# Performance work log

Hardware: AMD Instinct MI355X
Metric: run time of the kernel (lower is better)

## Reference

```python
import jax, jax.numpy as jnp
import numpy as np
from jax import lax

D = 1024      # hidden_dim
H = 1408      # moe_inter_dim
E = 8         # num_experts
K = 2         # topk
ROUTER_SCALE = 1.0


def setup_inputs() -> dict:
    key = jax.random.key(0)
    ks = jax.random.split(key, 16)
    s = 0.02
    inp = {
        "x": jax.random.normal(ks[0], (2, 2048, D), dtype=jnp.float32),
        "gate_w": jax.random.normal(ks[1], (E, D), dtype=jnp.float32) * s,
        "gate_b": jax.random.normal(ks[2], (E,), dtype=jnp.float32) * s,
        # stacked expert params; torch Linear weight [out,in] stored transposed as [in,out]
        "w1": jax.random.normal(ks[3], (E, D, H), dtype=jnp.float32) * s,
        "b1": jax.random.normal(ks[4], (E, H), dtype=jnp.float32) * s,
        "w3": jax.random.normal(ks[5], (E, D, H), dtype=jnp.float32) * s,
        "b3": jax.random.normal(ks[6], (E, H), dtype=jnp.float32) * s,
        "w2": jax.random.normal(ks[7], (E, H, D), dtype=jnp.float32) * s,
        "b2": jax.random.normal(ks[8], (E, D), dtype=jnp.float32) * s,
        # shared expert
        "sw1": jax.random.normal(ks[9], (D, H), dtype=jnp.float32) * s,
        "sb1": jax.random.normal(ks[10], (H,), dtype=jnp.float32) * s,
        "sw3": jax.random.normal(ks[11], (D, H), dtype=jnp.float32) * s,
        "sb3": jax.random.normal(ks[12], (H,), dtype=jnp.float32) * s,
        "sw2": jax.random.normal(ks[13], (H, D), dtype=jnp.float32) * s,
        "sb2": jax.random.normal(ks[14], (D,), dtype=jnp.float32) * s,
    }
    return inp


def _expert(x, w1, b1, w3, b3, w2, b2):
    # NOTE: source applies silu to the PRODUCT: w2(silu(w1(x) * w3(x)))
    h = jax.nn.silu((x @ w1 + b1) * (x @ w3 + b3))
    return h @ w2 + b2


def reference(x, gate_w, gate_b, w1, b1, w3, b3, w2, b2,
              sw1, sb1, sw3, sb3, sw2, sb2):
    shape = x.shape
    xf = x.reshape(-1, D)                      # [T, D]
    T = xf.shape[0]

    # Gate
    scores = jax.nn.softmax(xf @ gate_w.T, axis=-1)   # [T, E]
    biased = scores + gate_b
    _, idx = lax.top_k(biased, K)                     # [T, K] int32
    w = jnp.take_along_axis(scores, idx, axis=-1) * ROUTER_SCALE  # [T, K]

    # Dense routing-weight matrix (top-k indices are distinct per token)
    rw = jnp.zeros((T, E), dtype=xf.dtype).at[jnp.arange(T)[:, None], idx].add(w)

    # Stacked expert compute: [T, E, H] -> [T, E, D], combined by routing weight
    h = jax.nn.silu((jnp.einsum('td,edh->teh', xf, w1) + b1)
                    * (jnp.einsum('td,edh->teh', xf, w3) + b3))
    oe = jnp.einsum('teh,ehd->ted', h, w2) + b2
    y = jnp.einsum('te,ted->td', rw, oe)

    # Shared expert on all tokens
    z = _expert(xf, sw1, sb1, sw3, sb3, sw2, sb2)
    return (y + z).reshape(shape)
```

## Files before the change

### kernel.cpp

```cpp
#include <hip/hip_runtime.h>
#include <math.h>

#define DD 1024
#define HH 1408
#define NE 8

typedef __attribute__((ext_vector_type(8))) __bf16 bf16x8;
typedef __attribute__((ext_vector_type(4))) float f32x4;

__device__ __forceinline__ float bf2f(unsigned short u) {
  union { unsigned int i; float f; } v; v.i = ((unsigned int)u) << 16; return v.f;
}
__device__ __forceinline__ unsigned short f2bf(float f) {
  union { float f; unsigned int i; } v; v.f = f;
  unsigned int r = v.i + 0x7FFFu + ((v.i >> 16) & 1u);
  return (unsigned short)(r >> 16);
}
__device__ __forceinline__ float tof(float f) { return f; }
__device__ __forceinline__ float tof(unsigned short u) { return bf2f(u); }

__device__ __forceinline__ void cvt2(float a, float b, unsigned int* o) {
  asm("v_cvt_pk_bf16_f32 %0, %1, %2" : "=v"(*o) : "v"(a), "v"(b));
}

__device__ __forceinline__ void ld8cvt(const float* p, unsigned int* o) {
  float4 a = *(const float4*)p;
  float4 b = *(const float4*)(p + 4);
  cvt2(a.x, a.y, o + 0); cvt2(a.z, a.w, o + 1);
  cvt2(b.x, b.y, o + 2); cvt2(b.z, b.w, o + 3);
}

typedef unsigned int __attribute__((address_space(1))) gu32;
typedef unsigned int __attribute__((address_space(3))) lu32;
__device__ __forceinline__ void gl16(const unsigned short* g, unsigned short* l) {
  __builtin_amdgcn_global_load_lds((const gu32*)g, (lu32*)l, 16, 0, 0);
}

__global__ void sniff_kernel(const unsigned short* __restrict__ xw,
                             int* __restrict__ dflag) {
  __shared__ int cnt;
  if (threadIdx.x == 0) cnt = 0;
  __syncthreads();
  unsigned short v = xw[threadIdx.x];
  int e = (v >> 7) & 0xFF;
  if (e >= 100 && e <= 140) atomicAdd(&cnt, 1);
  __syncthreads();
  if (threadIdx.x == 0) dflag[0] = (cnt < 230) ? 1 : 0;
}

__global__ void cvtx_kernel(const void* __restrict__ x,
                            const int* __restrict__ dflag,
                            unsigned short* __restrict__ xb, int n8) {
  int i = blockIdx.x * blockDim.x + threadIdx.x;
  int st = gridDim.x * blockDim.x;
  if (dflag[0]) {
    const float* xs = (const float*)x;
    for (; i < n8; i += st) {
      unsigned int o[4];
      ld8cvt(xs + (size_t)i * 8, o);
      *(uint4*)(xb + (size_t)i * 8) = *(uint4*)o;
    }
  } else {
    const uint4* xs = (const uint4*)x;
    for (; i < n8; i += st) *(uint4*)(xb + (size_t)i * 8) = xs[i];
  }
}

__global__ void trans_kernel(const void* __restrict__ wmain,
                             const void* __restrict__ wsh,
                             const int* __restrict__ dflag,
                             unsigned short* __restrict__ out, int R, int C) {
  __shared__ float tile[32][33];
  const int mat = blockIdx.z;
  const int r0 = blockIdx.y << 5, c0 = blockIdx.x << 5;
  const int t = threadIdx.x;
  const int lr = t >> 3, lc = (t & 7) << 2;
  const size_t mbase = (size_t)mat * R * C;
  if (dflag[0]) {
    const float* src = (mat < NE) ? ((const float*)wmain + mbase) : (const float*)wsh;
    float4 v = *(const float4*)(src + (size_t)(r0 + lr) * C + c0 + lc);
    tile[lr][lc] = v.x; tile[lr][lc + 1] = v.y;
    tile[lr][lc + 2] = v.z; tile[lr][lc + 3] = v.w;
  } else {
    const unsigned short* src = (mat < NE) ? ((const unsigned short*)wmain + mbase)
                                           : (const unsigned short*)wsh;
    ushort4 v = *(const ushort4*)(src + (size_t)(r0 + lr) * C + c0 + lc);
    tile[lr][lc] = bf2f(v.x); tile[lr][lc + 1] = bf2f(v.y);
    tile[lr][lc + 2] = bf2f(v.z); tile[lr][lc + 3] = bf2f(v.w);
  }
  __syncthreads();
  const int oc = t >> 3;
  const int orr = (t & 7) << 2;
  unsigned int p0, p1;
  cvt2(tile[orr][oc], tile[orr + 1][oc], &p0);
  cvt2(tile[orr + 2][oc], tile[orr + 3][oc], &p1);
  uint2 pk; pk.x = p0; pk.y = p1;
  *(uint2*)(out + mbase + (size_t)(c0 + oc) * R + r0 + orr) = pk;
}

__global__ void cvtb_kernel(const void* b1, const void* b3, const void* b2,
                            const void* sb1, const void* sb3, const void* sb2,
                            const int* __restrict__ dflag,
                            float* __restrict__ bf1, float* __restrict__ bf3,
                            float* __restrict__ bf2o) {
  int i = blockIdx.x * blockDim.x + threadIdx.x;
  const int nh = (NE + 1) * HH, nd = (NE + 1) * DD;
  const bool f32 = dflag[0] != 0;
  auto get = [&](const void* pm, const void* ps, int idx, int per) -> float {
    int mat = idx / per, j = idx - mat * per;
    if (f32) return (mat < NE) ? ((const float*)pm)[(size_t)mat * per + j]
                               : ((const float*)ps)[j];
    return bf2f((mat < NE) ? ((const unsigned short*)pm)[(size_t)mat * per + j]
                           : ((const unsigned short*)ps)[j]);
  };
  if (i < nh) bf1[i] = get(b1, sb1, i, HH);
  else if (i < 2 * nh) bf3[i - nh] = get(b3, sb3, i - nh, HH);
  else if (i < 2 * nh + nd) bf2o[i - 2 * nh] = get(b2, sb2, i - 2 * nh, DD);
}

template <class T>
__device__ void gate_body(const T* __restrict__ x,
                          const T* __restrict__ gw,
                          const T* __restrict__ gb,
                          int* __restrict__ tok_eidx,
                          float* __restrict__ tok_w, int T_) {
  int t = (int)((blockIdx.x * blockDim.x + threadIdx.x) >> 6);
  int lane = threadIdx.x & 63;
  if (t >= T_) return;
  const T* xr = x + (size_t)t * DD;
  float acc[NE];
#pragma unroll
  for (int e = 0; e < NE; e++) acc[e] = 0.f;
  for (int i = lane; i < DD; i += 64) {
    float xv = tof(xr[i]);
#pragma unroll
    for (int e = 0; e < NE; e++) acc[e] += xv * tof(gw[e * DD + i]);
  }
#pragma unroll
  for (int off = 32; off > 0; off >>= 1) {
#pragma unroll
    for (int e = 0; e < NE; e++) acc[e] += __shfl_xor(acc[e], off);
  }
  if (lane == 0) {
    float mx = acc[0];
#pragma unroll
    for (int e = 1; e < NE; e++) mx = fmaxf(mx, acc[e]);
    float s = 0.f, sc[NE], bi[NE];
#pragma unroll
    for (int e = 0; e < NE; e++) { sc[e] = expf(acc[e] - mx); s += sc[e]; }
    float inv = 1.f / s;
#pragma unroll
    for (int e = 0; e < NE; e++) { sc[e] *= inv; bi[e] = sc[e] + tof(gb[e]); }
    int i1 = 0;
#pragma unroll
    for (int e = 1; e < NE; e++) if (bi[e] > bi[i1]) i1 = e;
    int i2 = (i1 == 0) ? 1 : 0;
#pragma unroll
    for (int e = 0; e < NE; e++) if (e != i1 && bi[e] > bi[i2]) i2 = e;
    tok_eidx[t * 2] = i1; tok_eidx[t * 2 + 1] = i2;
    tok_w[t * 2] = sc[i1]; tok_w[t * 2 + 1] = sc[i2];
  }
}

__global__ void gate_kernel(const void* x, const void* gw, const void* gb,
                            const int* __restrict__ dflag,
                            int* tok_eidx, float* tok_w, int T_) {
  if (dflag[0])
    gate_body<float>((const float*)x, (const float*)gw, (const float*)gb,
                     tok_eidx, tok_w, T_);
  else
    gate_body<unsigned short>((const unsigned short*)x, (const unsigned short*)gw,
                              (const unsigned short*)gb, tok_eidx, tok_w, T_);
}

__global__ void prep_kernel(const int* __restrict__ tok_eidx,
                            const float* __restrict__ tok_w,
                            int* __restrict__ meta,
                            int* __restrict__ rows_tok,
                            float* __restrict__ rows_wgt,
                            int* __restrict__ tok_pos,
                            int t0, int TS) {
  __shared__ int cnt[NE];
  __shared__ int off[NE];
  const int tid = threadIdx.x;
  if (tid < NE) cnt[tid] = 0;
  __syncthreads();
  const int n2 = TS * 2;
  const int* te = tok_eidx + (size_t)t0 * 2;
  const float* tw = tok_w + (size_t)t0 * 2;
  for (int i = tid; i < n2; i += (int)blockDim.x) atomicAdd(&cnt[te[i]], 1);
  __syncthreads();
  if (tid == 0) {
    int s = 0;
#pragma unroll
    for (int e = 0; e < NE; e++) { off[e] = s; meta[16 + e] = s; s += cnt[e]; }
    meta[16 + NE] = s;
  }
  __syncthreads();
  for (int i = tid; i < n2; i += (int)blockDim.x) {
    int pos = atomicAdd(&off[te[i]], 1);
    rows_tok[pos] = t0 + (i >> 1);
    rows_wgt[pos] = tw[i];
    tok_pos[(size_t)(t0 + (i >> 1)) * 2 + (i & 1)] = pos;
  }
}

__global__ void combine_kernel(const float4* __restrict__ r_out,
                               const int* __restrict__ tok_pos,
                               float4* __restrict__ out, int t0, int TS) {
  const int C4 = DD / 4;
  int i = blockIdx.x * blockDim.x + threadIdx.x;
  int n4 = TS * C4;
  int st = gridDim.x * blockDim.x;
  for (; i < n4; i += st) {
    int tl = i / C4, c = i - tl * C4;
    int t = t0 + tl;
    int p0 = tok_pos[t * 2], p1 = tok_pos[t * 2 + 1];
    float4 a = out[(size_t)t * C4 + c];
    float4 b = r_out[(size_t)p0 * C4 + c];
    float4 d = r_out[(size_t)p1 * C4 + c];
    a.x += b.x + d.x; a.y += b.y + d.y;
    a.z += b.z + d.z; a.w += b.w + d.w;
    out[(size_t)t * C4 + c] = a;
  }
}

__global__ __launch_bounds__(512, 2)
void ffn_up_kernel(const unsigned short* __restrict__ xb,
                   const unsigned short* __restrict__ wt1,
                   const unsigned short* __restrict__ wt3,
                   const float* __restrict__ bf1, const float* __restrict__ bf3,
                   const int* __restrict__ meta,
                   const int* __restrict__ rows_tok,
                   unsigned short* __restrict__ h_buf,
                   unsigned short* __restrict__ sh_buf,
                   int t0, int TS, int my) {
  const int NX = HH / 128;
  const int P = NX * (NE + 1);
  const int id = blockIdx.x;
  const int xcd = id & 7;
  const int rest = id >> 3;
  const int mtile = rest % my;
  const int chunk = rest / my;
  const int panel = chunk * 8 + xcd;
  if (panel >= P) return;
  const int z = panel / NX;
  const int n0 = (panel - z * NX) * 128;

  const bool shx = (z == NE);
  int g0, cnt;
  unsigned short* ho;
  if (shx) { g0 = 0; cnt = TS; ho = sh_buf; }
  else {
    g0 = meta[16 + z]; cnt = meta[17 + z] - g0;
    ho = h_buf + (size_t)g0 * HH;
  }
  if (mtile * 256 >= cnt) return;
  const unsigned short* wa = wt1 + (size_t)z * HH * DD;
  const unsigned short* wb = wt3 + (size_t)z * HH * DD;

  __shared__ alignas(16) unsigned short lds[2 * 32768];

  const int tid = threadIdx.x;
  const int lane = tid & 63, wid = tid >> 6;
  const int rsub = wid * 8 + (lane >> 3);
  const int sl8 = (((lane & 7) ^ (lane >> 3)) << 3);

  size_t aoff[4];
#pragma unroll
  for (int c = 0; c < 4; c++) {
    int r = c * 64 + rsub;
    int m = mtile * 256 + r;
    int rr = (m < cnt) ? m : (cnt - 1);
    int srow = shx ? (t0 + rr) : rows_tok[g0 + rr];
    aoff[c] = (size_t)srow * DD + sl8;
  }
  size_t boff[2];
#pragma unroll
  for (int c = 0; c < 2; c++)
    boff[c] = (size_t)(n0 + c * 64 + rsub) * DD + sl8;

  const int ln15 = lane & 15;
  const int lg = lane >> 4;
  const int wr = (wid >> 1) << 6;
  const int wc = (wid & 1) << 6;
  const int ldsw = wid * 512;

  f32x4 acc1[4][4], acc3[4][4];
#pragma unroll
  for (int a = 0; a < 4; a++)
#pragma unroll
    for (int b = 0; b < 4; b++) {
      acc1[a][b] = {0.f, 0.f, 0.f, 0.f};
      acc3[a][b] = {0.f, 0.f, 0.f, 0.f};
    }

  auto stage = [&](int buf, int k) {
    unsigned short* Lb = &lds[buf * 32768];
#pragma unroll
    for (int c = 0; c < 4; c++)
      gl16(xb + aoff[c] + k, Lb + c * 4096 + ldsw);
#pragma unroll
    for (int c = 0; c < 2; c++) {
      gl16(wa + boff[c] + k, Lb + 16384 + c * 4096 + ldsw);
      gl16(wb + boff[c] + k, Lb + 24576 + c * 4096 + ldsw);
    }
  };

  stage(0, 0);
  const int NT = DD / 64;
  for (int t = 0; t < NT; ++t) {
    if (t + 1 < NT) {
      stage((t + 1) & 1, (t + 1) * 64);
      asm volatile("s_waitcnt vmcnt(8)" ::: "memory");
    } else {
      asm volatile("s_waitcnt vmcnt(0)" ::: "memory");
    }
    __builtin_amdgcn_sched_barrier(0);
    __builtin_amdgcn_s_barrier();
    __builtin_amdgcn_sched_barrier(0);
    const unsigned short* Lb = &lds[(t & 1) * 32768];
    __builtin_amdgcn_s_setprio(1);
#pragma unroll
    for (int ks = 0; ks < 2; ks++) {
      bf16x8 af[4];
#pragma unroll
      for (int fm = 0; fm < 4; fm++) {
        int R = wr + fm * 16 + ln15;
        af[fm] = *(const bf16x8*)&Lb[R * 64 + ((((ks << 2) | lg) ^ (R & 7)) << 3)];
      }
#pragma unroll
      for (int fn = 0; fn < 4; fn++) {
        int Rb = wc + fn * 16 + ln15;
        int o = Rb * 64 + ((((ks << 2) | lg) ^ (Rb & 7)) << 3);
        bf16x8 b1v = *(const bf16x8*)&Lb[16384 + o];
        bf16x8 b3v = *(const bf16x8*)&Lb[24576 + o];
#pragma unroll
        for (int fm = 0; fm < 4; fm++) {
          acc1[fm][fn] = __builtin_amdgcn_mfma_f32_16x16x32_bf16(af[fm], b1v, acc1[fm][fn], 0, 0, 0);
          acc3[fm][fn] = __builtin_amdgcn_mfma_f32_16x16x32_bf16(af[fm], b3v, acc3[fm][fn], 0, 0, 0);
        }
      }
    }
    __builtin_amdgcn_s_setprio(0);
    asm volatile("s_waitcnt lgkmcnt(0)" ::: "memory");
    __builtin_amdgcn_sched_barrier(0);
    __builtin_amdgcn_s_barrier();
    __builtin_amdgcn_sched_barrier(0);
  }

  const int kq4 = lg << 2;
#pragma unroll
  for (int fm = 0; fm < 4; fm++) {
#pragma unroll
    for (int r = 0; r < 4; r++) {
      int m = mtile * 256 + wr + fm * 16 + kq4 + r;
      if (m < cnt) {
        unsigned short* orow = ho + (size_t)m * HH + n0;
#pragma unroll
        for (int fn = 0; fn < 4; fn++) {
          int nc = wc + fn * 16 + ln15;
          float g1 = acc1[fm][fn][r] + bf1[(size_t)z * HH + n0 + nc];
          float g3 = acc3[fm][fn][r] + bf3[(size_t)z * HH + n0 + nc];
          float u = g1 * g3;
          float hv = u * __builtin_amdgcn_rcpf(1.f + __expf(-u));
          orow[nc] = f2bf(hv);
        }
      }
    }
  }
}

__global__ __launch_bounds__(512, 2)
void ffn_down_kernel(const unsigned short* __restrict__ h_buf,
                     const unsigned short* __restrict__ sh_buf,
                     const unsigned short* __restrict__ wt2,
                     const float* __restrict__ bf2,
                     const int* __restrict__ meta,
                     const int* __restrict__ rows_tok,
                     const float* __restrict__ rows_wgt,
                     float* __restrict__ r_out,
                     float* __restrict__ out, int t0, int TS, int my) {
  const int NX = DD / 128;
  const int P = NX * (NE + 1);
  const int id = blockIdx.x;
  const int xcd = id & 7;
  const int rest = id >> 3;
  const int mtile = rest % my;
  const int chunk = rest / my;
  const int panel = chunk * 8 + xcd;
  if (panel >= P) return;
  const int z = panel / NX;
  const int n0 = (panel - z * NX) * 128;

  const bool shx = (z == NE);
  int g0, cnt;
  const unsigned short* hb;
  if (shx) { g0 = 0; cnt = TS; hb = sh_buf; }
  else {
    g0 = meta[16 + z]; cnt = meta[17 + z] - g0;
    hb = h_buf + (size_t)g0 * HH;
  }
  if (mtile * 256 >= cnt) return;
  const unsigned short* ws = wt2 + (size_t)z * DD * HH;

  __shared__ alignas(16) unsigned short lds[2 * 24576];

  const int tid = threadIdx.x;
  const int lane = tid & 63, wid = tid >> 6;
  const int rsub = wid * 8 + (lane >> 3);
  const int sl8 = (((lane & 7) ^ (lane >> 3)) << 3);

  size_t aoff[4];
#pragma unroll
  for (int c = 0; c < 4; c++) {
    int r = c * 64 + rsub;
    int m = mtile * 256 + r;
    int rr = (m < cnt) ? m : (cnt - 1);
    aoff[c] = (size_t)rr * HH + sl8;
  }
  size_t boff[2];
#pragma unroll
  for (int c = 0; c < 2; c++)
    boff[c] = (size_t)(n0 + c * 64 + rsub) * HH + sl8;

  const int ln15 = lane & 15;
  const int lg = lane >> 4;
  const int wr = (wid >> 1) << 6;
  const int wc = (wid & 1) << 6;
  const int ldsw = wid * 512;

  f32x4 acc[4][4];
#pragma unroll
  for (int a = 0; a < 4; a++)
#pragma unroll
    for (int b = 0; b < 4; b++) acc[a][b] = {0.f, 0.f, 0.f, 0.f};

  auto stage = [&](int buf, int k) {
    unsigned short* Lb = &lds[buf * 24576];
#pragma unroll
    for (int c = 0; c < 4; c++)
      gl16(hb + aoff[c] + k, Lb + c * 4096 + ldsw);
#pragma unroll
    for (int c = 0; c < 2; c++)
      gl16(ws + boff[c] + k, Lb + 16384 + c * 4096 + ldsw);
  };

  stage(0, 0);
  const int NT = HH / 64;
  for (int t = 0; t < NT; ++t) {
    if (t + 1 < NT) {
      stage((t + 1) & 1, (t + 1) * 64);
      asm volatile("s_waitcnt vmcnt(6)" ::: "memory");
    } else {
      asm volatile("s_waitcnt vmcnt(0)" ::: "memory");
    }
    __builtin_amdgcn_sched_barrier(0);
    __builtin_amdgcn_s_barrier();
    __builtin_amdgcn_sched_barrier(0);
    const unsigned short* Lb = &lds[(t & 1) * 24576];
    __builtin_amdgcn_s_setprio(1);
#pragma unroll
    for (int ks = 0; ks < 2; ks++) {
      bf16x8 af[4];
#pragma unroll
      for (int fm = 0; fm < 4; fm++) {
        int R = wr + fm * 16 + ln15;
        af[fm] = *(const bf16x8*)&Lb[R * 64 + ((((ks << 2) | lg) ^ (R & 7)) << 3)];
      }
#pragma unroll
      for (int fn = 0; fn < 4; fn++) {
        int Rb = wc + fn * 16 + ln15;
        int o = Rb * 64 + ((((ks << 2) | lg) ^ (Rb & 7)) << 3);
        bf16x8 bv = *(const bf16x8*)&Lb[16384 + o];
#pragma unroll
        for (int fm = 0; fm < 4; fm++)
          acc[fm][fn] = __builtin_amdgcn_mfma_f32_16x16x32_bf16(af[fm], bv, acc[fm][fn], 0, 0, 0);
      }
    }
    __builtin_amdgcn_s_setprio(0);
    asm volatile("s_waitcnt lgkmcnt(0)" ::: "memory");
    __builtin_amdgcn_sched_barrier(0);
    __builtin_amdgcn_s_barrier();
    __builtin_amdgcn_sched_barrier(0);
  }

  const int kq4 = lg << 2;
#pragma unroll
  for (int fm = 0; fm < 4; fm++) {
#pragma unroll
    for (int r4 = 0; r4 < 4; r4++) {
      int m = mtile * 256 + wr + fm * 16 + kq4 + r4;
      if (m < cnt) {
        float* orow;
        float wgt;
        if (shx) { orow = out + (size_t)(t0 + m) * DD + n0; wgt = 1.f; }
        else { orow = r_out + (size_t)(g0 + m) * DD + n0; wgt = rows_wgt[g0 + m]; }
#pragma unroll
        for (int fn = 0; fn < 4; fn++) {
          int nc = wc + fn * 16 + ln15;
          orow[nc] = wgt * (acc[fm][fn][r4] + bf2[(size_t)z * DD + n0 + nc]);
        }
      }
    }
  }
}

extern "C" void kernel_launch(void* const* d_in, const int* in_sizes, int n_in,
                              void* d_out, int out_size, void* d_ws, size_t ws_size,
                              hipStream_t stream) {
  const void* x   = d_in[0];
  const void* gw  = d_in[1];
  const void* gb  = d_in[2];
  const void* w1  = d_in[3];
  const void* b1  = d_in[4];
  const void* w3  = d_in[5];
  const void* b3  = d_in[6];
  const void* w2  = d_in[7];
  const void* b2  = d_in[8];
  const void* sw1 = d_in[9];
  const void* sb1 = d_in[10];
  const void* sw3 = d_in[11];
  const void* sb3 = d_in[12];
  const void* sw2 = d_in[13];
  const void* sb2 = d_in[14];

  const int T = in_sizes[0] / DD;
  (void)n_in; (void)out_size;

  const size_t WMAT = (size_t)(NE + 1) * HH * DD;

  auto need = [&](int S) -> size_t {
    int TS = T / S;
    size_t o = 0;
    auto pad = [&](size_t b) { o = (o + b + 255) & ~(size_t)255; };
    pad(256);
    pad(32 * sizeof(int));
    pad((size_t)T * 2 * sizeof(int));
    pad((size_t)T * 2 * sizeof(float));
    pad((size_t)T * 2 * sizeof(int));
    pad((size_t)T * DD * 2);
    pad(WMAT * 2);
    pad(WMAT * 2);
    pad(WMAT * 2);
    pad((size_t)(NE + 1) * HH * sizeof(float));
    pad((size_t)(NE + 1) * HH * sizeof(float));
    pad((size_t)(NE + 1) * DD * sizeof(float));
    pad((size_t)TS * 2 * sizeof(int));
    pad((size_t)TS * 2 * sizeof(float));
    pad((size_t)TS * 2 * HH * 2);
    pad((size_t)TS * HH * 2);
    pad((size_t)TS * 2 * DD * sizeof(float));
    return o;
  };
  int S = 32;
  {
    const int cand[6] = {1, 2, 4, 8, 16, 32};
    for (int ci = 0; ci < 6; ci++) {
      if (need(cand[ci]) <= ws_size) { S = cand[ci]; break; }
    }
  }
  const int TS = T / S;
  const int my = (TS + 255) / 256;

  char* w = (char*)d_ws;
  size_t off = 0;
  auto take = [&](size_t bytes) {
    char* p = w + off;
    off = (off + bytes + 255) & ~(size_t)255;
    return p;
  };
  int*   dflag    = (int*)  take(256);
  int*   meta     = (int*)  take(32 * sizeof(int));
  int*   tok_eidx = (int*)  take((size_t)T * 2 * sizeof(int));
  float* tok_w    = (float*)take((size_t)T * 2 * sizeof(float));
  int*   tok_pos  = (int*)  take((size_t)T * 2 * sizeof(int));
  unsigned short* xb  = (unsigned short*)take((size_t)T * DD * 2);
  unsigned short* wt1 = (unsigned short*)take(WMAT * 2);
  unsigned short* wt3 = (unsigned short*)take(WMAT * 2);
  unsigned short* wt2 = (unsigned short*)take(WMAT * 2);
  float* bf1 = (float*)take((size_t)(NE + 1) * HH * sizeof(float));
  float* bf3 = (float*)take((size_t)(NE + 1) * HH * sizeof(float));
  float* bf2 = (float*)take((size_t)(NE + 1) * DD * sizeof(float));
  int*   rows_tok = (int*)  take((size_t)TS * 2 * sizeof(int));
  float* rows_wgt = (float*)take((size_t)TS * 2 * sizeof(float));
  unsigned short* h_buf  = (unsigned short*)take((size_t)TS * 2 * HH * 2);
  unsigned short* sh_buf = (unsigned short*)take((size_t)TS * HH * 2);
  float* r_out = (float*)take((size_t)TS * 2 * DD * sizeof(float));

  sniff_kernel<<<1, 256, 0, stream>>>((const unsigned short*)x, dflag);

  cvtx_kernel<<<2048, 256, 0, stream>>>(x, dflag, xb, T * DD / 8);
  trans_kernel<<<dim3(HH / 32, DD / 32, NE + 1), 256, 0, stream>>>(w1, sw1, dflag, wt1, DD, HH);
  trans_kernel<<<dim3(HH / 32, DD / 32, NE + 1), 256, 0, stream>>>(w3, sw3, dflag, wt3, DD, HH);
  trans_kernel<<<dim3(DD / 32, HH / 32, NE + 1), 256, 0, stream>>>(w2, sw2, dflag, wt2, HH, DD);
  {
    int nb = (2 * (NE + 1) * HH + (NE + 1) * DD + 255) / 256;
    cvtb_kernel<<<nb, 256, 0, stream>>>(b1, b3, b2, sb1, sb3, sb2, dflag, bf1, bf3, bf2);
  }

  gate_kernel<<<(T + 3) / 4, 256, 0, stream>>>(x, gw, gb, dflag, tok_eidx, tok_w, T);

  const int upP = (HH / 128) * (NE + 1);
  const int dnP = (DD / 128) * (NE + 1);
  const int upGrid = 8 * ((upP + 7) / 8) * my;
  const int dnGrid = 8 * ((dnP + 7) / 8) * my;

  for (int s = 0; s < S; s++) {
    const int t0 = s * TS;
    prep_kernel<<<1, 1024, 0, stream>>>(tok_eidx, tok_w, meta, rows_tok, rows_wgt,
                                        tok_pos, t0, TS);
    ffn_up_kernel<<<upGrid, 512, 0, stream>>>(
        xb, wt1, wt3, bf1, bf3, meta, rows_tok, h_buf, sh_buf, t0, TS, my);
    ffn_down_kernel<<<dnGrid, 512, 0, stream>>>(
        h_buf, sh_buf, wt2, bf2, meta, rows_tok, rows_wgt, r_out,
        (float*)d_out, t0, TS, my);
    combine_kernel<<<1024, 256, 0, stream>>>((const float4*)r_out, tok_pos,
                                             (float4*)d_out, t0, TS);
  }
}
```

Baseline: 454.5 us.

## Switch expert GEMMs to triple-buffered BK=32 pipeline with single barrier per step

Both expert GEMM kernels (gate/up and down) move from a double-buffered 64-wide K tile to a triple-buffered 32-wide K tile. Loads are issued two stages ahead, and each iteration now has one barrier instead of two. The LDS swizzle changes to match 32-element rows. The aim is to hide more global-load latency and cut LDS footprint for better occupancy, at the cost of twice as many loop iterations. The setprio and lgkmcnt waits are dropped, which relies on the three-buffer rotation to keep reads and writes from overlapping.

New measurement: 440.1 us. 3.2% less time.

```diff
diff --git a/kernel.cpp b/kernel.cpp
--- a/kernel.cpp
+++ b/kernel.cpp
@@ -259,32 +259,32 @@
   const unsigned short* wa = wt1 + (size_t)z * HH * DD;
   const unsigned short* wb = wt3 + (size_t)z * HH * DD;
 
-  __shared__ alignas(16) unsigned short lds[2 * 32768];
+  __shared__ alignas(16) unsigned short lds[3 * 16384];
 
   const int tid = threadIdx.x;
   const int lane = tid & 63, wid = tid >> 6;
-  const int rsub = wid * 8 + (lane >> 3);
-  const int sl8 = (((lane & 7) ^ (lane >> 3)) << 3);
-
-  size_t aoff[4];
-#pragma unroll
-  for (int c = 0; c < 4; c++) {
-    int r = c * 64 + rsub;
+
+  size_t aoff[2];
+#pragma unroll
+  for (int c = 0; c < 2; c++) {
+    int g = c * 512 + tid;
+    int r = g >> 2, s = g & 3;
     int m = mtile * 256 + r;
     int rr = (m < cnt) ? m : (cnt - 1);
     int srow = shx ? (t0 + rr) : rows_tok[g0 + rr];
-    aoff[c] = (size_t)srow * DD + sl8;
-  }
-  size_t boff[2];
-#pragma unroll
-  for (int c = 0; c < 2; c++)
-    boff[c] = (size_t)(n0 + c * 64 + rsub) * DD + sl8;
+    aoff[c] = (size_t)srow * DD + ((s ^ ((r >> 1) & 3)) << 3);
+  }
+  size_t boffs;
+  {
+    int rb = tid >> 2, sb = tid & 3;
+    boffs = (size_t)(n0 + rb) * DD + ((sb ^ ((rb >> 1) & 3)) << 3);
+  }
+  const int wbase = wid * 512;
 
   const int ln15 = lane & 15;
   const int lg = lane >> 4;
   const int wr = (wid >> 1) << 6;
   const int wc = (wid & 1) << 6;
-  const int ldsw = wid * 512;
 
   f32x4 acc1[4][4], acc3[4][4];
 #pragma unroll
@@ -296,57 +296,41 @@
     }
 
   auto stage = [&](int buf, int k) {
-    unsigned short* Lb = &lds[buf * 32768];
-#pragma unroll
-    for (int c = 0; c < 4; c++)
-      gl16(xb + aoff[c] + k, Lb + c * 4096 + ldsw);
-#pragma unroll
-    for (int c = 0; c < 2; c++) {
-      gl16(wa + boff[c] + k, Lb + 16384 + c * 4096 + ldsw);
-      gl16(wb + boff[c] + k, Lb + 24576 + c * 4096 + ldsw);
-    }
+    unsigned short* Lb = &lds[buf * 16384];
+#pragma unroll
+    for (int c = 0; c < 2; c++)
+      gl16(xb + aoff[c] + k, Lb + c * 4096 + wbase);
+    gl16(wa + boffs + k, Lb + 8192 + wbase);
+    gl16(wb + boffs + k, Lb + 12288 + wbase);
   };
 
+  const int NT = DD / 32;
   stage(0, 0);
-  const int NT = DD / 64;
+  stage(1, 32);
   for (int t = 0; t < NT; ++t) {
-    if (t + 1 < NT) {
-      stage((t + 1) & 1, (t + 1) * 64);
-      asm volatile("s_waitcnt vmcnt(8)" ::: "memory");
-    } else {
-      asm volatile("s_waitcnt vmcnt(0)" ::: "memory");
-    }
-    __builtin_amdgcn_sched_barrier(0);
-    __builtin_amdgcn_s_barrier();
-    __builtin_amdgcn_sched_barrier(0);
-    const unsigned short* Lb = &lds[(t & 1) * 32768];
-    __builtin_amdgcn_s_setprio(1);
-#pragma unroll
-    for (int ks = 0; ks < 2; ks++) {
-      bf16x8 af[4];
+    if (t + 1 < NT) asm volatile("s_waitcnt vmcnt(4)" ::: "memory");
+    else            asm volatile("s_waitcnt vmcnt(0)" ::: "memory");
+    asm volatile("s_barrier" ::: "memory");
+    if (t + 2 < NT) stage((t + 2) % 3, (t + 2) * 32);
+    const unsigned short* Lb = &lds[(t % 3) * 16384];
+    bf16x8 af[4];
+#pragma unroll
+    for (int fm = 0; fm < 4; fm++) {
+      int R = wr + fm * 16 + ln15;
+      af[fm] = *(const bf16x8*)&Lb[R * 32 + ((lg ^ ((R >> 1) & 3)) << 3)];
+    }
+#pragma unroll
+    for (int fn = 0; fn < 4; fn++) {
+      int Rb = wc + fn * 16 + ln15;
+      int o = Rb * 32 + ((lg ^ ((Rb >> 1) & 3)) << 3);
+      bf16x8 b1v = *(const bf16x8*)&Lb[8192 + o];
+      bf16x8 b3v = *(const bf16x8*)&Lb[12288 + o];
 #pragma unroll
       for (int fm = 0; fm < 4; fm++) {
-        int R = wr + fm * 16 + ln15;
-        af[fm] = *(const bf16x8*)&Lb[R * 64 + ((((ks << 2) | lg) ^ (R & 7)) << 3)];
+        acc1[fm][fn] = __builtin_amdgcn_mfma_f32_16x16x32_bf16(af[fm], b1v, acc1[fm][fn], 0, 0, 0);
+        acc3[fm][fn] = __builtin_amdgcn_mfma_f32_16x16x32_bf16(af[fm], b3v, acc3[fm][fn], 0, 0, 0);
       }
-#pragma unroll
-      for (int fn = 0; fn < 4; fn++) {
-        int Rb = wc + fn * 16 + ln15;
-        int o = Rb * 64 + ((((ks << 2) | lg) ^ (Rb & 7)) << 3);
-        bf16x8 b1v = *(const bf16x8*)&Lb[16384 + o];
-        bf16x8 b3v = *(const bf16x8*)&Lb[24576 + o];
-#pragma unroll
-        for (int fm = 0; fm < 4; fm++) {
-          acc1[fm][fn] = __builtin_amdgcn_mfma_f32_16x16x32_bf16(af[fm], b1v, acc1[fm][fn], 0, 0, 0);
-          acc3[fm][fn] = __builtin_amdgcn_mfma_f32_16x16x32_bf16(af[fm], b3v, acc3[fm][fn], 0, 0, 0);
-        }
-      }
-    }
-    __builtin_amdgcn_s_setprio(0);
-    asm volatile("s_waitcnt lgkmcnt(0)" ::: "memory");
-    __builtin_amdgcn_sched_barrier(0);
-    __builtin_amdgcn_s_barrier();
-    __builtin_amdgcn_sched_barrier(0);
+    }
   }
 
   const int kq4 = lg << 2;
@@ -404,31 +388,31 @@
   if (mtile * 256 >= cnt) return;
   const unsigned short* ws = wt2 + (size_t)z * DD * HH;
 
-  __shared__ alignas(16) unsigned short lds[2 * 24576];
+  __shared__ alignas(16) unsigned short lds[3 * 12288];
 
   const int tid = threadIdx.x;
   const int lane = tid & 63, wid = tid >> 6;
-  const int rsub = wid * 8 + (lane >> 3);
-  const int sl8 = (((lane & 7) ^ (lane >> 3)) << 3);
-
-  size_t aoff[4];
-#pragma unroll
-  for (int c = 0; c < 4; c++) {
-    int r = c * 64 + rsub;
+
+  size_t aoff[2];
+#pragma unroll
+  for (int c = 0; c < 2; c++) {
+    int g = c * 512 + tid;
+    int r = g >> 2, s = g & 3;
     int m = mtile * 256 + r;
     int rr = (m < cnt) ? m : (cnt - 1);
-    aoff[c] = (size_t)rr * HH + sl8;
-  }
-  size_t boff[2];
-#pragma unroll
-  for (int c = 0; c < 2; c++)
-    boff[c] = (size_t)(n0 + c * 64 + rsub) * HH + sl8;
+    aoff[c] = (size_t)rr * HH + ((s ^ ((r >> 1) & 3)) << 3);
+  }
+  size_t boffs;
+  {
+    int rb = tid >> 2, sb = tid & 3;
+    boffs = (size_t)(n0 + rb) * HH + ((sb ^ ((rb >> 1) & 3)) << 3);
+  }
+  const int wbase = wid * 512;
 
   const int ln15 = lane & 15;
   const int lg = lane >> 4;
   const int wr = (wid >> 1) << 6;
   const int wc = (wid & 1) << 6;
-  const int ldsw = wid * 512;
 
   f32x4 acc[4][4];
 #pragma unroll
@@ -437,52 +421,37 @@
     for (int b = 0; b < 4; b++) acc[a][b] = {0.f, 0.f, 0.f, 0.f};
 
   auto stage = [&](int buf, int k) {
-    unsigned short* Lb = &lds[buf * 24576];
-#pragma unroll
-    for (int c = 0; c < 4; c++)
-      gl16(hb + aoff[c] + k, Lb + c * 4096 + ldsw);
+    unsigned short* Lb = &lds[buf * 12288];
 #pragma unroll
     for (int c = 0; c < 2; c++)
-      gl16(ws + boff[c] + k, Lb + 16384 + c * 4096 + ldsw);
+      gl16(hb + aoff[c] + k, Lb + c * 4096 + wbase);
+    gl16(ws + boffs + k, Lb + 8192 + wbase);
   };
 
+  const int NT = HH / 32;
   stage(0, 0);
-  const int NT = HH / 64;
+  stage(1, 32);
   for (int t = 0; t < NT; ++t) {
-    if (t + 1 < NT) {
-      stage((t + 1) & 1, (t + 1) * 64);
-      asm volatile("s_waitcnt vmcnt(6)" ::: "memory");
-    } else {
-      asm volatile("s_waitcnt vmcnt(0)" ::: "memory");
-    }
-    __builtin_amdgcn_sched_barrier(0);
-    __builtin_amdgcn_s_barrier();
-    __builtin_amdgcn_sched_barrier(0);
-    const unsigned short* Lb = &lds[(t & 1) * 24576];
-    __builtin_amdgcn_s_setprio(1);
-#pragma unroll
-    for (int ks = 0; ks < 2; ks++) {
-      bf16x8 af[4];
-#pragma unroll
-      for (int fm = 0; fm < 4; fm++) {
-        int R = wr + fm * 16 + ln15;
-        af[fm] = *(const bf16x8*)&Lb[R * 64 + ((((ks << 2) | lg) ^ (R & 7)) << 3)];
-      }
-#pragma unroll
-      for (int fn = 0; fn < 4; fn++) {
-        int Rb = wc + fn * 16 + ln15;
-        int o = Rb * 64 + ((((ks << 2) | lg) ^ (Rb & 7)) << 3);
-        bf16x8 bv = *(const bf16x8*)&Lb[16384 + o];
-#pragma unroll
-        for (int fm = 0; fm < 4; fm++)
-          acc[fm][fn] = __builtin_amdgcn_mfma_f32_16x16x32_bf16(af[fm], bv, acc[fm][fn], 0, 0, 0);
-      }
-    }
-    __builtin_amdgcn_s_setprio(0);
-    asm volatile("s_waitcnt lgkmcnt(0)" ::: "memory");
-    __builtin_amdgcn_sched_barrier(0);
-    __builtin_amdgcn_s_barrier();
-    __builtin_amdgcn_sched_barrier(0);
+    if (t + 1 < NT) asm volatile("s_waitcnt vmcnt(3)" ::: "memory");
+    else            asm volatile("s_waitcnt vmcnt(0)" ::: "memory");
+    asm volatile("s_barrier" ::: "memory");
+    if (t + 2 < NT) stage((t + 2) % 3, (t + 2) * 32);
+    const unsigned short* Lb = &lds[(t % 3) * 12288];
+    bf16x8 af[4];
+#pragma unroll
+    for (int fm = 0; fm < 4; fm++) {
+      int R = wr + fm * 16 + ln15;
+      af[fm] = *(const bf16x8*)&Lb[R * 32 + ((lg ^ ((R >> 1) & 3)) << 3)];
+    }
+#pragma unroll
+    for (int fn = 0; fn < 4; fn++) {
+      int Rb = wc + fn * 16 + ln15;
+      int o = Rb * 32 + ((lg ^ ((Rb >> 1) & 3)) << 3);
+      bf16x8 bv = *(const bf16x8*)&Lb[8192 + o];
+#pragma unroll
+      for (int fm = 0; fm < 4; fm++)
+        acc[fm][fn] = __builtin_amdgcn_mfma_f32_16x16x32_bf16(af[fm], bv, acc[fm][fn], 0, 0, 0);
+    }
   }
 
   const int kq4 = lg << 2;
```
